# Kernel optimization log

Measured on AMD Instinct MI355X. Metric: run time of the kernel, lower is better.

## Reference

```python
import jax, jax.numpy as jnp
import numpy as np

T, B, I, H, NL = 512, 64, 1024, 1024, 2  # time, batch, input, hidden, layers


def setup_inputs() -> dict:
    key = jax.random.key(0)
    k0, k1, k2, k3, k4 = jax.random.split(key, 5)
    # xavier-uniform bound for W: [fan_in, 3*H]
    bound = float(np.sqrt(6.0 / (I + 3 * H)))
    x = jax.random.normal(k0, (T, B, I), jnp.float32)
    h0 = jax.random.normal(k1, (NL, B, H), jnp.float32) * 0.1  # initial hidden states
    W1 = jax.random.uniform(k2, (I, 3 * H), jnp.float32, -bound, bound)
    b1 = jnp.zeros((3 * H,), jnp.float32)
    W2 = jax.random.uniform(k3, (H, 3 * H), jnp.float32, -bound, bound)
    b2 = jnp.zeros((3 * H,), jnp.float32)
    L = jax.random.randint(k4, (B,), 0, T)  # per-example valid lengths
    return {"x": x, "h0": h0, "W1": W1, "b1": b1, "W2": W2, "b2": b2, "L": L}


def _lrn_layer(xs, h_init, W, b, L):
    # Hoist the input projection out of the time loop: same math as per-step mm.
    gates = jnp.einsum('tbi,ig->tbg', xs, W) + b          # [T, B, 3H]
    p, q, r = jnp.split(gates, 3, axis=-1)                 # each [T, B, H]
    # mask[t, b] = 1 if t < L[b] else 0 (keeps old state past sequence end)
    mask = (jnp.arange(xs.shape[0])[:, None] < L[None, :]).astype(xs.dtype)[:, :, None]

    def step(h, inp):
        pt, qt, rt, mt = inp
        i = jax.nn.sigmoid(pt + h)
        f = jax.nn.sigmoid(qt - h)
        nh = jnp.tanh(i * rt + f * h)
        nh = nh * mt + h * (1.0 - mt)
        return nh, nh

    h_last, out = jax.lax.scan(step, h_init, (p, q, r, mask))
    return out, h_last


def reference(x, h0, W1, b1, W2, b2, L):
    out1, h1 = _lrn_layer(x, h0[0], W1, b1, L)
    out2, h2 = _lrn_layer(out1, h0[1], W2, b2, L)   # dropout=0 -> identity between layers
    return out2, jnp.stack([h1, h2], axis=0)
```

## Files before the change

kernel.cpp:

```cpp
#include <hip/hip_runtime.h>

#define T_DIM 512
#define B_DIM 64
#define I_DIM 1024
#define H_DIM 1024
#define G3    3072
#define M_DIM (T_DIM * B_DIM)
#define K_DIM 1024
#define KT    16

typedef unsigned short u16;
typedef __bf16 bf16x8 __attribute__((ext_vector_type(8)));
typedef float  f32x4  __attribute__((ext_vector_type(4)));
typedef unsigned short u16x8 __attribute__((ext_vector_type(8)));
typedef unsigned short u16x4 __attribute__((ext_vector_type(4)));

__device__ __forceinline__ u16 f2bf(float x) {
  union { float f; unsigned u; } v; v.f = x;
  unsigned r = v.u + 0x7fffu + ((v.u >> 16) & 1u);
  return (u16)(r >> 16);
}
__device__ __forceinline__ float bf2f(u16 x) {
  union { unsigned u; float f; } v; v.u = ((unsigned)x) << 16;
  return v.f;
}

__global__ void build_offsets_kernel(const int* __restrict__ L, int* __restrict__ meta) {
  __shared__ int cnt[T_DIM];
  __shared__ int Ls[B_DIM];
  const int t = threadIdx.x;
  if (t < B_DIM) Ls[t] = L[t];
  __syncthreads();
  int n = 0;
  #pragma unroll 8
  for (int b = 0; b < B_DIM; ++b) n += (Ls[b] > t) ? 1 : 0;
  cnt[t] = n;
  __syncthreads();
  if (t == 0) {
    int acc = 0;
    for (int s = 0; s < T_DIM; ++s) { int c = cnt[s]; cnt[s] = acc; acc += c; }
    meta[T_DIM] = acc;
    meta[513] = acc;
    meta[514] = (acc + 511) & ~511;
  }
  __syncthreads();
  meta[t] = cnt[t];
}

__global__ void build_crow_kernel(const int* __restrict__ L, const int* __restrict__ meta,
                                  int* __restrict__ crow, int* __restrict__ crowT) {
  const int t = blockIdx.x;
  const int b = threadIdx.x;
  const bool valid = t < L[b];
  unsigned long long mask = __ballot(valid);
  const int rank = __popcll(mask & ((1ull << b) - 1ull));
  if (valid) {
    const int cr = meta[t] + rank;
    crow[(t << 6) + b] = cr;
    crowT[(b << 9) + t] = cr;
  }
}

__global__ void cast_gather_kernel(const float* __restrict__ in, const int* __restrict__ L,
                                   const int* __restrict__ crow, u16* __restrict__ out, int n8) {
  int idx = blockIdx.x * blockDim.x + threadIdx.x;
  int stride = gridDim.x * blockDim.x;
  for (int i = idx; i < n8; i += stride) {
    const int row = i >> 7;
    const int ch  = i & 127;
    const int b = row & 63, t = row >> 6;
    if (t >= L[b]) continue;
    const int cr = crow[row];
    const float4* p = (const float4*)(in + (size_t)row * 1024 + ch * 8);
    float4 a = p[0], bb = p[1];
    u16x8 o;
    o[0] = f2bf(a.x);  o[1] = f2bf(a.y);  o[2] = f2bf(a.z);  o[3] = f2bf(a.w);
    o[4] = f2bf(bb.x); o[5] = f2bf(bb.y); o[6] = f2bf(bb.z); o[7] = f2bf(bb.w);
    *(u16x8*)(out + (size_t)cr * 1024 + ch * 8) = o;
  }
}

__global__ void transpose_cast_kernel(const float* __restrict__ W1, const float* __restrict__ W2,
                                      u16* __restrict__ W1t, u16* __restrict__ W2t) {
  __shared__ float tile[32][33];
  const float* W = blockIdx.z ? W2 : W1;
  u16* Wt       = blockIdx.z ? W2t : W1t;
  int n0 = blockIdx.x * 32, k0 = blockIdx.y * 32;
  int tx = threadIdx.x, ty = threadIdx.y;
  #pragma unroll
  for (int dy = 0; dy < 32; dy += 8)
    tile[ty + dy][tx] = W[(size_t)(k0 + ty + dy) * G3 + n0 + tx];
  __syncthreads();
  #pragma unroll
  for (int dy = 0; dy < 32; dy += 8)
    Wt[(size_t)(n0 + ty + dy) * K_DIM + k0 + tx] = f2bf(tile[tx][ty + dy]);
}

__device__ __forceinline__ void gload_lds16(const void* g, void* l) {
  __builtin_amdgcn_global_load_lds(
      (const __attribute__((address_space(1))) void*)g,
      (__attribute__((address_space(3))) void*)l, 16, 0, 0);
}

__device__ __forceinline__ void stage_half(const u16* __restrict__ G, u16* lbuf,
                                           int rb, int k0, int w, int l) {
  const int cs   = (l & 7) ^ (l >> 3);
  const int rsub = l >> 3;
  #pragma unroll
  for (int r = 0; r < 2; ++r) {
    const int row0 = rb + r * 64 + w * 8;
    gload_lds16(G + (size_t)(row0 + rsub) * K_DIM + k0 + cs * 8,
                lbuf + (size_t)row0 * 64);
  }
}

__device__ __forceinline__ bf16x8 ldfrag(const u16* buf, int row, int ks, int fr, int g4) {
  const int slot = ((ks << 2) + g4) ^ (fr & 7);
  return *(const bf16x8*)(buf + (size_t)row * 64 + slot * 8);
}

__device__ __forceinline__ void read_a(const u16* buf, bf16x8 (&dst)[4][2],
                                       int rbase, int fr, int g4) {
  #pragma unroll
  for (int m = 0; m < 4; ++m) {
    dst[m][0] = ldfrag(buf, rbase + m * 16 + fr, 0, fr, g4);
    dst[m][1] = ldfrag(buf, rbase + m * 16 + fr, 1, fr, g4);
  }
}
__device__ __forceinline__ void read_b(const u16* buf, bf16x8 (&dst)[2][2],
                                       int rbase, int fr, int g4) {
  #pragma unroll
  for (int n = 0; n < 2; ++n) {
    dst[n][0] = ldfrag(buf, rbase + n * 16 + fr, 0, fr, g4);
    dst[n][1] = ldfrag(buf, rbase + n * 16 + fr, 1, fr, g4);
  }
}

#define BARRIER()  do { __builtin_amdgcn_s_barrier(); __builtin_amdgcn_sched_barrier(0); } while (0)
#define LGKM0()    do { asm volatile("s_waitcnt lgkmcnt(0)" ::: "memory"); __builtin_amdgcn_sched_barrier(0); } while (0)

#define MFMA_Q(ACC, AV, BV)                                                            \
  do {                                                                                 \
    __builtin_amdgcn_s_setprio(1);                                                     \
    _Pragma("unroll")                                                                  \
    for (int m = 0; m < 4; ++m)                                                        \
      _Pragma("unroll")                                                                \
      for (int n = 0; n < 2; ++n) {                                                    \
        ACC = __builtin_amdgcn_mfma_f32_16x16x32_bf16(AV[m][0], BV[n][0], ACC, 0, 0, 0); \
        ACC = __builtin_amdgcn_mfma_f32_16x16x32_bf16(AV[m][1], BV[n][1], ACC, 0, 0, 0); \
      }                                                                                \
    __builtin_amdgcn_s_setprio(0);                                                     \
  } while (0)

__global__ __launch_bounds__(512, 2) void gemm256_kernel(
    const u16* __restrict__ A, const u16* __restrict__ Bt,
    const float* __restrict__ bias, u16* __restrict__ C, int N,
    const int* __restrict__ meta) {
  __shared__ u16 As[2][256 * 64];
  __shared__ u16 Bs[2][256 * 64];
  const int tid = threadIdx.x;
  const int l  = tid & 63, w = tid >> 6;
  const int wm = w >> 2,  wn = w & 3;
  const int fr = l & 15,  g4 = l >> 4;

  const int ny   = meta[514] >> 8;
  const int nact = gridDim.x * ny;
  const int q    = nact >> 3;
  const int lin  = blockIdx.y * gridDim.x + blockIdx.x;
  const int idx  = lin >> 3;
  if (idx >= q) return;
  const int swz = (lin & 7) * q + idx;
  const int bx = swz % gridDim.x, by = swz / gridDim.x;
  const int bm = by * 256, bn = bx * 256;

  const u16* Ab = A  + (size_t)bm * K_DIM;
  const u16* Bb = Bt + (size_t)bn * K_DIM;

  stage_half(Ab, As[0], 0,   0,  w, l);
  stage_half(Ab, As[0], 128, 0,  w, l);
  stage_half(Bb, Bs[0], 0,   0,  w, l);
  stage_half(Bb, Bs[0], 128, 0,  w, l);
  stage_half(Ab, As[1], 0,   64, w, l);
  stage_half(Ab, As[1], 128, 64, w, l);
  stage_half(Bb, Bs[1], 0,   64, w, l);

  f32x4 acc[8][4] = {};
  bf16x8 av0[4][2], av1[4][2], bv0[2][2], bv1[2][2];

  for (int T = 0; T < KT - 1; ++T) {
    const u16* Ac = As[T & 1];
    const u16* Bc = Bs[T & 1];
    u16* Bn1 = Bs[(T + 1) & 1];
    u16* An2 = As[T & 1];        u16* Bn2 = Bs[T & 1];
    const int k1 = (T + 1) * 64, k2 = (T + 2) * 64;
    const bool st2 = (T + 2) < KT;

    asm volatile("s_waitcnt vmcnt(6)" ::: "memory");
    BARRIER();

    read_a(Ac, av0, wm * 128, fr, g4);
    read_b(Bc, bv0, wn * 64, fr, g4);
    stage_half(Bb, Bn1, 128, k1, w, l);
    LGKM0();

    MFMA_Q(acc[m][n], av0, bv0);
    read_b(Bc, bv1, wn * 64 + 32, fr, g4);
    LGKM0();

    MFMA_Q(acc[m][n + 2], av0, bv1);
    read_a(Ac, av1, wm * 128 + 64, fr, g4);
    LGKM0();
    BARRIER();

    if (st2) {
      stage_half(Ab, An2, 0,   k2, w, l);
      stage_half(Ab, An2, 128, k2, w, l);
      stage_half(Bb, Bn2, 0,   k2, w, l);
    }

    MFMA_Q(acc[m + 4][n + 2], av1, bv1);
    MFMA_Q(acc[m + 4][n],     av1, bv0);
  }

  {
    const u16* Ac = As[(KT - 1) & 1];
    const u16* Bc = Bs[(KT - 1) & 1];
    asm volatile("s_waitcnt vmcnt(0)" ::: "memory");
    BARRIER();
    #pragma unroll
    for (int m = 0; m < 4; ++m) {
      av0[m][0] = ldfrag(Ac, wm * 128 + m * 16 + fr, 0, fr, g4);
      av0[m][1] = ldfrag(Ac, wm * 128 + m * 16 + fr, 1, fr, g4);
      av1[m][0] = ldfrag(Ac, wm * 128 + (m + 4) * 16 + fr, 0, fr, g4);
      av1[m][1] = ldfrag(Ac, wm * 128 + (m + 4) * 16 + fr, 1, fr, g4);
    }
    #pragma unroll
    for (int n = 0; n < 2; ++n) {
      bv0[n][0] = ldfrag(Bc, wn * 64 + n * 16 + fr, 0, fr, g4);
      bv0[n][1] = ldfrag(Bc, wn * 64 + n * 16 + fr, 1, fr, g4);
      bv1[n][0] = ldfrag(Bc, wn * 64 + (n + 2) * 16 + fr, 0, fr, g4);
      bv1[n][1] = ldfrag(Bc, wn * 64 + (n + 2) * 16 + fr, 1, fr, g4);
    }
    LGKM0();
    MFMA_Q(acc[m][n],         av0, bv0);
    MFMA_Q(acc[m][n + 2],     av0, bv1);
    MFMA_Q(acc[m + 4][n + 2], av1, bv1);
    MFMA_Q(acc[m + 4][n],     av1, bv0);
    BARRIER();
  }

  float bb[4];
  #pragma unroll
  for (int j = 0; j < 4; ++j) bb[j] = bias[bn + wn * 64 + j * 16 + fr];

  u16* eb = (w < 4) ? ((u16*)As + (size_t)w * 8192)
                    : ((u16*)Bs + (size_t)(w - 4) * 8192);
  #pragma unroll
  for (int i = 0; i < 8; ++i)
    #pragma unroll
    for (int j = 0; j < 4; ++j)
      #pragma unroll
      for (int v = 0; v < 4; ++v) {
        const int row = i * 16 + g4 * 4 + v;
        const int col = j * 16 + fr;
        eb[row * 64 + (col ^ ((row & 12) << 2))] = f2bf(acc[i][j][v] + bb[j]);
      }
  LGKM0();
  #pragma unroll
  for (int c = 0; c < 16; ++c) {
    const int lrow = c * 8 + (l >> 3);
    const int lcol = (l & 7) * 8;
    u16x8 d = *(const u16x8*)&eb[lrow * 64 + (lcol ^ ((lrow & 12) << 2))];
    *(u16x8*)&C[(size_t)(bm + wm * 128 + lrow) * N + (bn + wn * 64 + lcol)] = d;
  }
}

__device__ __forceinline__ float stepf(float h, u16 gp, u16 gq, u16 gr) {
  float p = bf2f(gp), q = bf2f(gq), r = bf2f(gr);
  float ii = 1.f / (1.f + __expf(-(p + h)));
  float ff = 1.f / (1.f + __expf(-(q - h)));
  float u  = ii * r + ff * h;
  float e2 = __expf(2.f * u);
  return 1.f - 2.f / (e2 + 1.f);
}

#define SD 16

#define PRODUCE(CC)                                                            \
  do {                                                                         \
    u16 vp[SD], vq[SD], vr[SD];                                                \
    const int base_ = (CC) * SD;                                               \
    _Pragma("unroll")                                                          \
    for (int s_ = 0; s_ < SD; ++s_) {                                          \
      const u16* g_ = gates + (size_t)crs[base_ + s_] * G3 + (slice << 8) + p; \
      vp[s_] = g_[0]; vq[s_] = g_[H_DIM]; vr[s_] = g_[2 * H_DIM];              \
    }                                                                          \
    u16* slot_ = ring[(CC) & 1];                                               \
    _Pragma("unroll")                                                          \
    for (int s_ = 0; s_ < SD; ++s_) {                                          \
      u16x4 w4 = {vp[s_], vq[s_], vr[s_], (u16)0};                             \
      *(u16x4*)&slot_[(s_ * 256 + p) * 4] = w4;                                \
    }                                                                          \
  } while (0)

#define CONSUME(CC, PART)                                                      \
  do {                                                                         \
    const u16* slot_ = ring[(CC) & 1];                                         \
    const int base_ = (CC) * SD;                                               \
    u16x4 gg[SD];                                                              \
    _Pragma("unroll")                                                          \
    for (int s_ = 0; s_ < SD; ++s_)                                            \
      gg[s_] = *(const u16x4*)&slot_[(s_ * 256 + jl) * 4];                     \
    _Pragma("unroll")                                                          \
    for (int s_ = 0; s_ < SD; ++s_) {                                          \
      if (!(PART) || base_ + s_ < Lb) {                                        \
        h = stepf(h, gg[s_][0], gg[s_][1], gg[s_][2]);                         \
        if (OUT_BF16) out_bf[(size_t)crs[base_ + s_] * H_DIM + jg] = f2bf(h);  \
        else out_f[((size_t)(base_ + s_) * B_DIM + b) * H_DIM + jg] = h;       \
      }                                                                        \
    }                                                                          \
  } while (0)

template <int OUT_BF16>
__global__ __launch_bounds__(512) void scan_pc_kernel(
    const u16* __restrict__ gates,
    const float* __restrict__ h0,
    const int* __restrict__ L,
    const int* __restrict__ crowT,
    u16* __restrict__ out_bf,
    float* __restrict__ out_f,
    float* __restrict__ hlast) {
  __shared__ u16 ring[2][SD * 256 * 4];
  __shared__ int crs[T_DIM + SD];
  __shared__ float hbuf[256];
  const int b     = blockIdx.x >> 2;
  const int slice = blockIdx.x & 3;
  const int tid   = threadIdx.x;
  const int Lb    = L[b];
  for (int i = tid; i < T_DIM + SD; i += 512)
    crs[i] = (i < Lb) ? crowT[(b << 9) + i] : 0;
  __syncthreads();

  const int nch   = (Lb + SD - 1) / SD;
  const int nfull = Lb / SD;
  const int jl  = tid & 255;
  const int p   = jl;
  const int jg  = (slice << 8) + jl;
  const bool producer = tid >= 256;
  float h = h0[(b << 10) + jg];

  if (producer && nch > 0) PRODUCE(0);
  __syncthreads();

  #pragma unroll 1
  for (int c = 0; c < nch; ++c) {
    if (producer) {
      if (c + 1 < nch) PRODUCE(c + 1);
    } else {
      if (c < nfull) CONSUME(c, 0);
      else           CONSUME(c, 1);
    }
    __syncthreads();
  }

  if (!producer) {
    hlast[(size_t)b * H_DIM + jg] = h;
    if (!OUT_BF16) hbuf[jl] = h;
  }
  if (!OUT_BF16) {
    __syncthreads();
    const float hv = hbuf[jl];
    for (int t = Lb + (tid >> 8); t < T_DIM; t += 2)
      out_f[((size_t)t * B_DIM + b) * H_DIM + jg] = hv;
  }
}

extern "C" void kernel_launch(void* const* d_in, const int* in_sizes, int n_in,
                              void* d_out, int out_size, void* d_ws, size_t ws_size,
                              hipStream_t stream) {
  const float* x  = (const float*)d_in[0];
  const float* h0 = (const float*)d_in[1];
  const float* W1 = (const float*)d_in[2];
  const float* b1 = (const float*)d_in[3];
  const float* W2 = (const float*)d_in[4];
  const float* b2 = (const float*)d_in[5];
  const int*   L  = (const int*)d_in[6];

  float* out2 = (float*)d_out;
  float* hl   = out2 + (size_t)T_DIM * B_DIM * H_DIM;

  char* w = (char*)d_ws;
  u16* xb    = (u16*)(w);
  u16* W1t   = (u16*)(w + (size_t)67108864);
  u16* W2t   = (u16*)(w + (size_t)73400320);
  u16* gates = (u16*)(w + (size_t)79691776);
  u16* out1  = (u16*)(w + (size_t)281018368);
  int* meta  = (int*)(w + (size_t)348127232);
  int* crow  = (int*)(w + (size_t)348131328);
  int* crowT = (int*)(w + (size_t)348262400);

  build_offsets_kernel<<<1, 512, 0, stream>>>(L, meta);
  build_crow_kernel<<<T_DIM, 64, 0, stream>>>(L, meta, crow, crowT);
  cast_gather_kernel<<<2048, 256, 0, stream>>>(x, L, crow, xb, (T_DIM * B_DIM * I_DIM) / 8);
  transpose_cast_kernel<<<dim3(G3 / 32, K_DIM / 32, 2), dim3(32, 8), 0, stream>>>(
      W1, W2, W1t, W2t);

  gemm256_kernel<<<dim3(G3 / 256, M_DIM / 256), 512, 0, stream>>>(
      xb, W1t, b1, gates, G3, meta);
  scan_pc_kernel<1><<<B_DIM * 4, 512, 0, stream>>>(
      gates, h0, L, crowT, out1, nullptr, hl);

  gemm256_kernel<<<dim3(G3 / 256, M_DIM / 256), 512, 0, stream>>>(
      out1, W2t, b2, gates, G3, meta);
  scan_pc_kernel<0><<<B_DIM * 4, 512, 0, stream>>>(
      gates, h0 + B_DIM * H_DIM, L, crowT, nullptr, out2, hl + B_DIM * H_DIM);
}
```

Baseline: 397.0 us.

## Merge offset/crow build kernels, use fast exp2/rcp in scan step, hoist row loads

```diff
diff --git a/kernel.cpp b/kernel.cpp
--- a/kernel.cpp
+++ b/kernel.cpp
@@ -25,7 +25,9 @@
   return v.f;
 }
 
-__global__ void build_offsets_kernel(const int* __restrict__ L, int* __restrict__ meta) {
+__global__ __launch_bounds__(512) void build_all_kernel(
+    const int* __restrict__ L, int* __restrict__ meta,
+    int* __restrict__ crow, int* __restrict__ crowT) {
   __shared__ int cnt[T_DIM];
   __shared__ int Ls[B_DIM];
   const int t = threadIdx.x;
@@ -45,19 +47,16 @@
   }
   __syncthreads();
   meta[t] = cnt[t];
-}
-
-__global__ void build_crow_kernel(const int* __restrict__ L, const int* __restrict__ meta,
-                                  int* __restrict__ crow, int* __restrict__ crowT) {
-  const int t = blockIdx.x;
-  const int b = threadIdx.x;
-  const bool valid = t < L[b];
-  unsigned long long mask = __ballot(valid);
-  const int rank = __popcll(mask & ((1ull << b) - 1ull));
-  if (valid) {
-    const int cr = meta[t] + rank;
-    crow[(t << 6) + b] = cr;
-    crowT[(b << 9) + t] = cr;
+  const int off = cnt[t];
+  int rank = 0;
+  #pragma unroll 8
+  for (int b = 0; b < B_DIM; ++b) {
+    if (t < Ls[b]) {
+      const int cr = off + rank;
+      crow[(t << 6) + b] = cr;
+      crowT[(b << 9) + t] = cr;
+      ++rank;
+    }
   }
 }
 
@@ -275,13 +274,16 @@
   }
 }
 
+#define LOG2E  1.4426950408889634f
+#define LOG2E2 2.8853900817779268f
+
 __device__ __forceinline__ float stepf(float h, u16 gp, u16 gq, u16 gr) {
   float p = bf2f(gp), q = bf2f(gq), r = bf2f(gr);
-  float ii = 1.f / (1.f + __expf(-(p + h)));
-  float ff = 1.f / (1.f + __expf(-(q - h)));
+  float ii = __builtin_amdgcn_rcpf(1.f + exp2f((-(p + h)) * LOG2E));
+  float ff = __builtin_amdgcn_rcpf(1.f + exp2f((h - q) * LOG2E));
   float u  = ii * r + ff * h;
-  float e2 = __expf(2.f * u);
-  return 1.f - 2.f / (e2 + 1.f);
+  float e2 = exp2f(u * LOG2E2);
+  return 1.f - 2.f * __builtin_amdgcn_rcpf(e2 + 1.f);
 }
 
 #define SD 16
@@ -308,14 +310,17 @@
     const u16* slot_ = ring[(CC) & 1];                                         \
     const int base_ = (CC) * SD;                                               \
     u16x4 gg[SD];                                                              \
+    int crl[SD];                                                               \
     _Pragma("unroll")                                                          \
-    for (int s_ = 0; s_ < SD; ++s_)                                            \
+    for (int s_ = 0; s_ < SD; ++s_) {                                          \
       gg[s_] = *(const u16x4*)&slot_[(s_ * 256 + jl) * 4];                     \
+      crl[s_] = crs[base_ + s_];                                               \
+    }                                                                          \
     _Pragma("unroll")                                                          \
     for (int s_ = 0; s_ < SD; ++s_) {                                          \
       if (!(PART) || base_ + s_ < Lb) {                                        \
         h = stepf(h, gg[s_][0], gg[s_][1], gg[s_][2]);                         \
-        if (OUT_BF16) out_bf[(size_t)crs[base_ + s_] * H_DIM + jg] = f2bf(h);  \
+        if (OUT_BF16) out_bf[(size_t)crl[s_] * H_DIM + jg] = f2bf(h);          \
         else out_f[((size_t)(base_ + s_) * B_DIM + b) * H_DIM + jg] = h;       \
       }                                                                        \
     }                                                                          \
@@ -399,8 +404,7 @@
   int* crow  = (int*)(w + (size_t)348131328);
   int* crowT = (int*)(w + (size_t)348262400);
 
-  build_offsets_kernel<<<1, 512, 0, stream>>>(L, meta);
-  build_crow_kernel<<<T_DIM, 64, 0, stream>>>(L, meta, crow, crowT);
+  build_all_kernel<<<1, 512, 0, stream>>>(L, meta, crow, crowT);
   cast_gather_kernel<<<2048, 256, 0, stream>>>(x, L, crow, xb, (T_DIM * B_DIM * I_DIM) / 8);
   transpose_cast_kernel<<<dim3(G3 / 32, K_DIM / 32, 2), dim3(32, 8), 0, stream>>>(
       W1, W2, W1t, W2t);
```

New measurement: 379.9 us. -4.3%, faster.
